# Performance work log

Measured on AMD Instinct MI355X. Metric: run time of the kernel, lower is better.

## Reference

```python
import jax, jax.numpy as jnp
import numpy as np

GROUPS = 8
HEADS = 8
EPS = 1e-5


def setup_inputs() -> dict:
    key = jax.random.key(0)
    ks = jax.random.split(key, 4)
    B, C, T = 4, 512, 2048
    x = jax.random.normal(ks[0], (B, C, T), dtype=jnp.float32)
    gn_w = jnp.ones((C,), dtype=jnp.float32)
    gn_b = jnp.zeros((C,), dtype=jnp.float32)
    qkv_w = jax.random.normal(ks[1], (3 * C, C), dtype=jnp.float32) * (1.0 / np.sqrt(C))
    qkv_b = jnp.zeros((3 * C,), dtype=jnp.float32)
    proj_w = jax.random.normal(ks[2], (C, C), dtype=jnp.float32) * (1.0 / np.sqrt(C))
    proj_b = jnp.zeros((C,), dtype=jnp.float32)
    return {"x": x, "gn_w": gn_w, "gn_b": gn_b, "qkv_w": qkv_w,
            "qkv_b": qkv_b, "proj_w": proj_w, "proj_b": proj_b}


def reference(x, gn_w, gn_b, qkv_w, qkv_b, proj_w, proj_b):
    b, c, t = x.shape
    # GroupNorm over (channels_in_group, T)
    xg = x.reshape(b, GROUPS, c // GROUPS, t)
    mean = xg.mean(axis=(2, 3), keepdims=True)
    var = xg.var(axis=(2, 3), keepdims=True)
    h = ((xg - mean) * jax.lax.rsqrt(var + EPS)).reshape(b, c, t)
    h = h * gn_w[None, :, None] + gn_b[None, :, None]
    # 1x1 conv qkv: [b, 3c, t]
    qkv = jnp.einsum('oc,bct->bot', qkv_w, h) + qkv_b[None, :, None]
    # split into heads: legacy layout [b*H, 3*ch, t] -> q,k,v each [b*H, ch, t]
    ch = c // HEADS
    qkv = qkv.reshape(b * HEADS, 3 * ch, t)
    q, k, v = qkv[:, :ch], qkv[:, ch:2 * ch], qkv[:, 2 * ch:]
    scale = 1.0 / np.sqrt(np.sqrt(ch))
    weight = jnp.einsum('bct,bcs->bts', q * scale, k * scale)  # [bH, t, t]
    weight = jax.nn.softmax(weight.astype(jnp.float32), axis=-1).astype(q.dtype)
    a = jnp.einsum('bts,bcs->bct', weight, v).reshape(b, c, t)
    # 1x1 conv proj
    out = jnp.einsum('oc,bct->bot', proj_w, a) + proj_b[None, :, None]
    return x + out
```

## Files before the change

kernel.cpp:

```cpp
#include <hip/hip_runtime.h>


typedef __attribute__((ext_vector_type(8))) short short8;
typedef __attribute__((ext_vector_type(4))) float f32x4;
typedef __attribute__((ext_vector_type(16))) float f32x16;

#define T_DIM 2048
#define C_DIM 512
#define B_DIM 4

__device__ __forceinline__ float bf2f(ushort u) {
  union { unsigned int i; float f; } x; x.i = ((unsigned int)u) << 16; return x.f;
}
__device__ __forceinline__ ushort f2bf(float f) {
  union { float f; unsigned int i; } x; x.f = f;
  unsigned int i = x.i;
  return (ushort)((i + 0x7FFFu + ((i >> 16) & 1u)) >> 16);
}
__device__ __forceinline__ unsigned int cvtpk_bf16(float lo, float hi) {
  unsigned int r;
  asm("v_cvt_pk_bf16_f32 %0, %1, %2" : "=v"(r) : "v"(lo), "v"(hi));
  return r;
}
__device__ __forceinline__ float exp2_raw(float x) {
  float r;
  asm("v_exp_f32 %0, %1" : "=v"(r) : "v"(x));
  return r;
}
__device__ __forceinline__ void gl_lds16(const ushort* g, const ushort* l) {
  __builtin_amdgcn_global_load_lds(
      (const __attribute__((address_space(1))) unsigned int*)g,
      (__attribute__((address_space(3))) unsigned int*)l, 16, 0, 0);
}

#define KT_SCALE 0.1803368801f

__global__ __launch_bounds__(256) void prep_kernel(
    const float* __restrict__ qkv_w, ushort* __restrict__ wq,
    const float* __restrict__ proj_w, ushort* __restrict__ wp,
    const float* __restrict__ x, float2* __restrict__ part) {
  const int bi = blockIdx.x;
  const int tid = threadIdx.x;
  if (bi < 1024) {
    const float* s = (bi < 768) ? qkv_w : proj_w;
    ushort* d = (bi < 768) ? wq : wp;
    int i = ((bi < 768) ? bi : bi - 768) * 256 + tid;
    float4 v = ((const float4*)s)[i];
    ushort4 o;
    o.x = f2bf(v.x); o.y = f2bf(v.y); o.z = f2bf(v.z); o.w = f2bf(v.w);
    ((ushort4*)d)[i] = o;
    return;
  }
  const int pb = bi - 1024;
  const float4* p4 = (const float4*)x + (size_t)pb * 2048;
  float s = 0.f, ss = 0.f;
#pragma unroll
  for (int i = 0; i < 8; i++) {
    float4 v = p4[tid + i * 256];
    s += v.x + v.y + v.z + v.w;
    ss += v.x * v.x + v.y * v.y + v.z * v.z + v.w * v.w;
  }
  for (int off = 32; off; off >>= 1) {
    s += __shfl_xor(s, off, 64);
    ss += __shfl_xor(ss, off, 64);
  }
  __shared__ float rbuf[8];
  int w = tid >> 6, lane = tid & 63;
  if (lane == 0) { rbuf[w * 2] = s; rbuf[w * 2 + 1] = ss; }
  __syncthreads();
  if (tid == 0) {
    float S = 0.f, SS = 0.f;
#pragma unroll
    for (int i = 0; i < 4; i++) { S += rbuf[2 * i]; SS += rbuf[2 * i + 1]; }
    part[pb] = make_float2(S, SS);
  }
}

__global__ __launch_bounds__(256) void gn_apply_t_kernel(
    const float* __restrict__ x, const float* __restrict__ gw,
    const float* __restrict__ gb, const float2* __restrict__ part,
    ushort* __restrict__ ht) {
  __shared__ ushort tile[64][66];
  __shared__ float sst[2];
  const int b = blockIdx.z, gy = blockIdx.y, c0 = gy * 64, t0 = blockIdx.x * 64;
  const int tid = threadIdx.x;
  if (tid < 64) {
    float s = 0.f, ss = 0.f;
    if (tid < 16) {
      float2 p = part[(b * 8 + gy) * 16 + tid];
      s = p.x; ss = p.y;
    }
    for (int off = 8; off; off >>= 1) {
      s += __shfl_xor(s, off, 64);
      ss += __shfl_xor(ss, off, 64);
    }
    if (tid == 0) {
      float mean = s * (1.f / 131072.f);
      float var = ss * (1.f / 131072.f) - mean * mean;
      sst[0] = mean;
      sst[1] = rsqrtf(var + 1e-5f);
    }
  }
  __syncthreads();
  const float mean = sst[0], rstd = sst[1];
  {
    const int cc = tid >> 2, tc = (tid & 3) * 16;
    const int c = c0 + cc;
    float sc = rstd * gw[c];
    float bb = gb[c] - mean * sc;
    const float4* src = (const float4*)(x + ((size_t)b * 512 + c) * T_DIM + t0 + tc);
    unsigned int* dst = (unsigned int*)&tile[cc][tc];
#pragma unroll
    for (int q = 0; q < 4; q++) {
      float4 v = src[q];
      float a0 = v.x * sc + bb, a1 = v.y * sc + bb;
      float a2 = v.z * sc + bb, a3 = v.w * sc + bb;
      dst[2 * q] = (unsigned int)f2bf(a0) | ((unsigned int)f2bf(a1) << 16);
      dst[2 * q + 1] = (unsigned int)f2bf(a2) | ((unsigned int)f2bf(a3) << 16);
    }
  }
  __syncthreads();
  {
    const int tt = tid >> 2, ch = (tid & 3) * 16;
    union { uint4 v4[2]; ushort u[16]; } z;
#pragma unroll
    for (int j = 0; j < 16; j++) z.u[j] = tile[ch + j][tt];
    ushort* dst = ht + ((size_t)b * T_DIM + t0 + tt) * 512 + c0 + ch;
    *(uint4*)dst = z.v4[0];
    *(uint4*)(dst + 8) = z.v4[1];
  }
}

template <int MODE, int MF>
__global__ __launch_bounds__(256, 3) void gemm_bt_kernel(
    const ushort* __restrict__ Wb, const ushort* __restrict__ Bt,
    const float* __restrict__ bias, const float* __restrict__ xres,
    ushort* __restrict__ outb, float* __restrict__ outf,
    ushort* __restrict__ ktp, int M) {
  __shared__ ushort As[MF * 32 * 64];
  __shared__ ushort Bs[128 * 64];
  const int b = blockIdx.z;
  const int t0 = blockIdx.x * 128, o0 = blockIdx.y * (MF * 32);
  const int tid = threadIdx.x, lane = tid & 63, w = tid >> 6;
  const int li = lane & 15, g = lane >> 4;
  const int wm = (w >> 1) * (MF * 16), wn = (w & 1) * 64;
  const int r8 = tid >> 3, bl = tid & 7;
  const ushort* Bbase = Bt + (size_t)b * T_DIM * 512;

  f32x4 acc[MF][4];
#pragma unroll
  for (int m = 0; m < MF; m++)
#pragma unroll
    for (int n = 0; n < 4; n++) acc[m][n] = (f32x4){0.f, 0.f, 0.f, 0.f};

  for (int ks = 0; ks < 8; ks++) {
    const int k0 = ks * 64;
#pragma unroll
    for (int i = 0; i < 4; i++) {
      int row = i * 32 + r8;
      int sb = (bl ^ (row & 7)) << 3;
      if (i < MF)
        gl_lds16(Wb + (size_t)(o0 + row) * 512 + k0 + sb, As + row * 64 + bl * 8);
      gl_lds16(Bbase + (size_t)(t0 + row) * 512 + k0 + sb, Bs + row * 64 + bl * 8);
    }
    __syncthreads();
#pragma unroll
    for (int kk = 0; kk < 2; kk++) {
      short8 af[MF], bf[4];
#pragma unroll
      for (int m = 0; m < MF; m++)
        af[m] = *(const short8*)&As[(wm + m * 16 + li) * 64 +
                                    (((kk * 4 + g) ^ (li & 7)) << 3)];
#pragma unroll
      for (int n = 0; n < 4; n++)
        bf[n] = *(const short8*)&Bs[(wn + n * 16 + li) * 64 +
                                    (((kk * 4 + g) ^ (li & 7)) << 3)];
      __builtin_amdgcn_s_setprio(1);
#pragma unroll
      for (int m = 0; m < MF; m++)
#pragma unroll
        for (int n = 0; n < 4; n++)
          acc[m][n] = __builtin_amdgcn_mfma_f32_16x16x32_bf16(af[m], bf[n],
                                                              acc[m][n], 0, 0, 0);
      __builtin_amdgcn_s_setprio(0);
    }
    __syncthreads();
  }

  size_t obase = (size_t)b * M * T_DIM;
#pragma unroll
  for (int m = 0; m < MF; m++) {
    const int om = o0 + wm + m * 16;
    bool isK = false;
    int head = 0, rem0 = 0;
    if (MODE == 0) {
      head = om / 192;
      rem0 = om - head * 192;
      isK = (rem0 >= 64 && rem0 < 128);
    }
    if (MODE == 0 && isK) {
      const int d0 = rem0 - 64 + g * 4;
      const size_t ktbase = (size_t)(b * 8 + head) * T_DIM;
      float bv0 = bias[om + g * 4 + 0];
      float bv1 = bias[om + g * 4 + 1];
      float bv2 = bias[om + g * 4 + 2];
      float bv3 = bias[om + g * 4 + 3];
#pragma unroll
      for (int n = 0; n < 4; n++) {
        int t = t0 + wn + n * 16 + li;
        ushort4 kv;
        kv.x = f2bf(KT_SCALE * (acc[m][n][0] + bv0));
        kv.y = f2bf(KT_SCALE * (acc[m][n][1] + bv1));
        kv.z = f2bf(KT_SCALE * (acc[m][n][2] + bv2));
        kv.w = f2bf(KT_SCALE * (acc[m][n][3] + bv3));
        *(ushort4*)(ktp + (ktbase + t) * 64 + d0) = kv;
      }
    } else {
#pragma unroll
      for (int r = 0; r < 4; r++) {
        int o = om + g * 4 + r;
        float bv = bias[o];
#pragma unroll
        for (int n = 0; n < 4; n++) {
          int t = t0 + wn + n * 16 + li;
          float v = acc[m][n][r] + bv;
          size_t idx = obase + (size_t)o * T_DIM + t;
          if (MODE == 0) outb[idx] = f2bf(v);
          else outf[idx] = v + xres[idx];
        }
      }
    }
  }
}

__global__ __launch_bounds__(256, 4) void attn_part_kernel(
    const ushort* __restrict__ qkv, const ushort* __restrict__ Ktg,
    ushort* __restrict__ opart, float* __restrict__ lpart) {
  __shared__ ushort SH[16384];
  const int bh = blockIdx.x, b = bh >> 3, hh = bh & 7;
  const int ttile = blockIdx.y;
  const int t0 = ttile * 128;
  const int shalf = blockIdx.z;
  const int tid = threadIdx.x, lane = tid & 63, w = tid >> 6;
  const int tl = lane & 31, hi = lane >> 5;
  const size_t base = ((size_t)b * 1536 + hh * 192) * (size_t)T_DIM;
  const ushort* Qp = qkv + base;
  const ushort* Vp = qkv + base + (size_t)128 * T_DIM + shalf * 1024;
  const ushort* Kp = Ktg + (size_t)bh * T_DIM * 64 + (size_t)shalf * 1024 * 64;
  const int tcol = t0 + w * 32 + tl;

  short8 qb[4];
#pragma unroll
  for (int kc = 0; kc < 4; kc++) {
    union { short8 s; ushort u[8]; } tmp;
#pragma unroll
    for (int j = 0; j < 8; j++)
      tmp.u[j] = Qp[(size_t)(kc * 16 + hi * 8 + j) * T_DIM + tcol];
    qb[kc] = tmp.s;
  }

  const int srow = lane >> 3;
  const int sblk = (lane & 7) ^ srow;

  const ushort* kg = Kp + (size_t)(w * 16 + srow) * 64 + sblk * 8;
  const ushort* vg = Vp + (size_t)(w * 16 + srow) * T_DIM + sblk * 8;
  const int ldW = w * 1024;

  f32x16 zv;
#pragma unroll
  for (int r = 0; r < 16; r++) zv[r] = 0.f;
  f32x16 oacc0, oacc1;
#pragma unroll
  for (int r = 0; r < 16; r++) { oacc0[r] = 0.f; oacc1[r] = 0.f; }
  float lsum = 0.f;

  gl_lds16(kg, SH + ldW);
  gl_lds16(kg + 512, SH + ldW + 512);
  gl_lds16(vg, SH + 8192 + ldW);
  gl_lds16(vg + 8 * T_DIM, SH + 8192 + ldW + 512);
  kg += 4096;
  vg += 64;

#define CHUNK(BUF, PF)                                                        \
  {                                                                           \
    __syncthreads();                                                          \
    if (PF) {                                                                 \
      gl_lds16(kg, SH + ((BUF) ^ 1) * 4096 + ldW);                            \
      gl_lds16(kg + 512, SH + ((BUF) ^ 1) * 4096 + ldW + 512);                \
      gl_lds16(vg, SH + 8192 + ((BUF) ^ 1) * 4096 + ldW);                     \
      gl_lds16(vg + 8 * T_DIM, SH + 8192 + ((BUF) ^ 1) * 4096 + ldW + 512);   \
      kg += 4096;                                                             \
      vg += 64;                                                               \
    }                                                                         \
    const ushort* kb = SH + (BUF) * 4096;                                     \
    const ushort* vb = SH + 8192 + (BUF) * 4096;                              \
    f32x16 s0, s1;                                                            \
    __builtin_amdgcn_s_setprio(1);                                            \
    _Pragma("unroll") for (int kc = 0; kc < 4; kc++) {                        \
      const int bo = (((kc * 2 + hi) ^ (tl & 7)) << 3);                       \
      short8 ak0 = *(const short8*)&kb[tl * 64 + bo];                         \
      short8 ak1 = *(const short8*)&kb[(32 + tl) * 64 + bo];                  \
      s0 = __builtin_amdgcn_mfma_f32_32x32x16_bf16(ak0, qb[kc],               \
                                                   kc == 0 ? zv : s0, 0, 0, 0);\
      s1 = __builtin_amdgcn_mfma_f32_32x32x16_bf16(ak1, qb[kc],               \
                                                   kc == 0 ? zv : s1, 0, 0, 0);\
    }                                                                         \
    __builtin_amdgcn_s_setprio(0);                                            \
    _Pragma("unroll") for (int r = 0; r < 16; r++) {                          \
      s0[r] = exp2_raw(s0[r]);                                                \
      s1[r] = exp2_raw(s1[r]);                                                \
    }                                                                         \
    {                                                                         \
      float a0 = (s0[0] + s0[1]) + (s0[2] + s0[3]);                           \
      float a1 = (s0[4] + s0[5]) + (s0[6] + s0[7]);                           \
      float a2 = (s0[8] + s0[9]) + (s0[10] + s0[11]);                         \
      float a3 = (s0[12] + s0[13]) + (s0[14] + s0[15]);                       \
      float b0 = (s1[0] + s1[1]) + (s1[2] + s1[3]);                           \
      float b1 = (s1[4] + s1[5]) + (s1[6] + s1[7]);                           \
      float b2 = (s1[8] + s1[9]) + (s1[10] + s1[11]);                         \
      float b3 = (s1[12] + s1[13]) + (s1[14] + s1[15]);                       \
      lsum += ((a0 + a1) + (a2 + a3)) + ((b0 + b1) + (b2 + b3));              \
    }                                                                         \
    unsigned int pw[2][8];                                                    \
    _Pragma("unroll") for (int p = 0; p < 8; p++) {                           \
      pw[0][p] = cvtpk_bf16(s0[2 * p], s0[2 * p + 1]);                        \
      pw[1][p] = cvtpk_bf16(s1[2 * p], s1[2 * p + 1]);                        \
    }                                                                         \
    short8 bp[4];                                                             \
    _Pragma("unroll") for (int kc = 0; kc < 4; kc++) {                        \
      const int n = kc >> 1, q = (kc & 1) * 4;                                \
      union { short8 s; unsigned int wv[4]; } bu;                             \
      _Pragma("unroll") for (int h = 0; h < 2; h++) {                         \
        unsigned int P0 = pw[n][q + h];                                       \
        unsigned int P1 = pw[n][q + 2 + h];                                   \
        asm volatile("v_permlane32_swap_b32 %0, %1" : "+v"(P0), "+v"(P1));    \
        bu.wv[h] = P0;                                                        \
        bu.wv[2 + h] = P1;                                                    \
      }                                                                       \
      bp[kc] = bu.s;                                                          \
    }                                                                         \
    __builtin_amdgcn_s_setprio(1);                                            \
    _Pragma("unroll") for (int kc = 0; kc < 4; kc++) {                        \
      const int bo = (((kc * 2 + hi) ^ (tl & 7)) << 3);                       \
      short8 av0 = *(const short8*)&vb[tl * 64 + bo];                         \
      short8 av1 = *(const short8*)&vb[(32 + tl) * 64 + bo];                  \
      oacc0 = __builtin_amdgcn_mfma_f32_32x32x16_bf16(av0, bp[kc], oacc0,     \
                                                      0, 0, 0);               \
      oacc1 = __builtin_amdgcn_mfma_f32_32x32x16_bf16(av1, bp[kc], oacc1,     \
                                                      0, 0, 0);               \
    }                                                                         \
    __builtin_amdgcn_s_setprio(0);                                            \
  }

  for (int cc = 0; cc < 8; cc++) {
    CHUNK(0, true);
    CHUNK(1, cc < 7);
  }
#undef CHUNK

  const int pidx = (bh * 16 + ttile) * 2 + shalf;
  ushort* op = opart + (size_t)pidx * 8192;
#pragma unroll
  for (int r = 0; r < 16; r++) {
    int crow = (r & 3) + 8 * (r >> 2) + 4 * hi;
    op[crow * 128 + w * 32 + tl] = f2bf(oacc0[r]);
    op[(32 + crow) * 128 + w * 32 + tl] = f2bf(oacc1[r]);
  }
  float lrow = lsum + __shfl_xor(lsum, 32);
  if (hi == 0) lpart[(size_t)pidx * 128 + w * 32 + tl] = lrow;
}

__global__ __launch_bounds__(256) void combine_kernel(
    const ushort* __restrict__ opart, const float* __restrict__ lpart,
    ushort* __restrict__ at) {
  __shared__ float invl[128];
  __shared__ ushort tile[128][66];
  const int bh = blockIdx.x, ttile = blockIdx.y, b = bh >> 3, hh = bh & 7;
  const int tid = threadIdx.x;
  const size_t pb = (size_t)(bh * 16 + ttile) * 2;
  const float* l0 = lpart + pb * 128;
  if (tid < 128) invl[tid] = 1.f / (l0[tid] + l0[128 + tid]);
  __syncthreads();
  {
    const int c = tid & 63, seg = tid >> 6;
    const ushort* r0 = opart + pb * 8192 + c * 128 + seg * 32;
    union { uint4 v[4]; ushort u[32]; } x0, x1;
#pragma unroll
    for (int j = 0; j < 4; j++) {
      x0.v[j] = *(const uint4*)(r0 + j * 8);
      x1.v[j] = *(const uint4*)(r0 + 8192 + j * 8);
    }
#pragma unroll
    for (int j = 0; j < 32; j++) {
      int t = seg * 32 + j;
      tile[t][c] = f2bf((bf2f(x0.u[j]) + bf2f(x1.u[j])) * invl[t]);
    }
  }
  __syncthreads();
  {
    const int t = tid >> 1, ch = (tid & 1) * 32;
    union { uint4 v[4]; ushort u[32]; } z;
#pragma unroll
    for (int j = 0; j < 32; j++) z.u[j] = tile[t][ch + j];
    uint4* dst = (uint4*)(at + ((size_t)b * T_DIM + ttile * 128 + t) * 512 +
                          hh * 64 + ch);
#pragma unroll
    for (int j = 0; j < 4; j++) dst[j] = z.v[j];
  }
}

extern "C" void kernel_launch(void* const* d_in, const int* in_sizes, int n_in,
                              void* d_out, int out_size, void* d_ws,
                              size_t ws_size, hipStream_t stream) {
  const float* x = (const float*)d_in[0];
  const float* gn_w = (const float*)d_in[1];
  const float* gn_b = (const float*)d_in[2];
  const float* qkv_w = (const float*)d_in[3];
  const float* qkv_b = (const float*)d_in[4];
  const float* proj_w = (const float*)d_in[5];
  const float* proj_b = (const float*)d_in[6];
  float* out = (float*)d_out;

  char* ws = (char*)d_ws;
  float2* part = (float2*)ws;
  ushort* ht_bf = (ushort*)(ws + 8192);
  ushort* at_bf = ht_bf;
  ushort* qkv_bf = (ushort*)(ws + 8192 + 8388608);
  ushort* wq_bf = (ushort*)(ws + 8192 + 8388608 + 25165824);
  ushort* wp_bf = (ushort*)(ws + 8192 + 8388608 + 25165824 + 1572864);
  ushort* kt_bf = (ushort*)(ws + 8192 + 8388608 + 25165824 + 1572864 + 524288);
  ushort* op_bf = (ushort*)(ws + 8192 + 8388608 + 25165824 + 1572864 + 524288 +
                            8388608);
  float* lp_f = (float*)(ws + 8192 + 8388608 + 25165824 + 1572864 + 524288 +
                         8388608 + 16777216);

  prep_kernel<<<1536, 256, 0, stream>>>(qkv_w, wq_bf, proj_w, wp_bf, x, part);
  gn_apply_t_kernel<<<dim3(32, 8, 4), 256, 0, stream>>>(x, gn_w, gn_b, part, ht_bf);
  gemm_bt_kernel<0, 4><<<dim3(16, 12, 4), 256, 0, stream>>>(
      wq_bf, ht_bf, qkv_b, nullptr, qkv_bf, nullptr, kt_bf, 1536);
  attn_part_kernel<<<dim3(32, 16, 2), 256, 0, stream>>>(qkv_bf, kt_bf, op_bf, lp_f);
  combine_kernel<<<dim3(32, 16), 256, 0, stream>>>(op_bf, lp_f, at_bf);
  gemm_bt_kernel<1, 2><<<dim3(16, 8, 4), 256, 0, stream>>>(
      wp_bf, at_bf, proj_b, x, nullptr, out, nullptr, 512);
}
```

Before: 96.97 us.

## Software-pipeline QK^T of next chunk with softmax and PV of previous chunk

Restructures the attention inner loop so that each iteration computes the S=K·Q MFMAs for chunk C, then runs exp, row sum, bf16 packing and the PV MFMAs for chunk C-1. V gets a triple-buffered LDS ring so the previous chunk's V stays valid while the next one is prefetched. The aim is to overlap MFMA work with the exp and permlane VALU work. In exchange it holds two sets of score accumulators live, which raises register pressure, and it enlarges LDS, so launch bounds drop from 4 to 3 blocks per CU.

```diff
diff --git a/kernel.cpp b/kernel.cpp
--- a/kernel.cpp
+++ b/kernel.cpp
@@ -233,10 +233,10 @@
   }
 }
 
-__global__ __launch_bounds__(256, 4) void attn_part_kernel(
+__global__ __launch_bounds__(256, 3) void attn_part_kernel(
     const ushort* __restrict__ qkv, const ushort* __restrict__ Ktg,
     ushort* __restrict__ opart, float* __restrict__ lpart) {
-  __shared__ ushort SH[16384];
+  __shared__ ushort SH[20480];
   const int bh = blockIdx.x, b = bh >> 3, hh = bh & 7;
   const int ttile = blockIdx.y;
   const int t0 = ttile * 128;
@@ -273,6 +273,7 @@
 #pragma unroll
   for (int r = 0; r < 16; r++) { oacc0[r] = 0.f; oacc1[r] = 0.f; }
   float lsum = 0.f;
+  f32x16 sA0, sA1, sB0, sB1;
 
   gl_lds16(kg, SH + ldW);
   gl_lds16(kg + 512, SH + ldW + 512);
@@ -281,50 +282,27 @@
   kg += 4096;
   vg += 64;
 
-#define CHUNK(BUF, PF)                                                        \
+#define SMPV(C, S)                                                            \
   {                                                                           \
-    __syncthreads();                                                          \
-    if (PF) {                                                                 \
-      gl_lds16(kg, SH + ((BUF) ^ 1) * 4096 + ldW);                            \
-      gl_lds16(kg + 512, SH + ((BUF) ^ 1) * 4096 + ldW + 512);                \
-      gl_lds16(vg, SH + 8192 + ((BUF) ^ 1) * 4096 + ldW);                     \
-      gl_lds16(vg + 8 * T_DIM, SH + 8192 + ((BUF) ^ 1) * 4096 + ldW + 512);   \
-      kg += 4096;                                                             \
-      vg += 64;                                                               \
-    }                                                                         \
-    const ushort* kb = SH + (BUF) * 4096;                                     \
-    const ushort* vb = SH + 8192 + (BUF) * 4096;                              \
-    f32x16 s0, s1;                                                            \
-    __builtin_amdgcn_s_setprio(1);                                            \
-    _Pragma("unroll") for (int kc = 0; kc < 4; kc++) {                        \
-      const int bo = (((kc * 2 + hi) ^ (tl & 7)) << 3);                       \
-      short8 ak0 = *(const short8*)&kb[tl * 64 + bo];                         \
-      short8 ak1 = *(const short8*)&kb[(32 + tl) * 64 + bo];                  \
-      s0 = __builtin_amdgcn_mfma_f32_32x32x16_bf16(ak0, qb[kc],               \
-                                                   kc == 0 ? zv : s0, 0, 0, 0);\
-      s1 = __builtin_amdgcn_mfma_f32_32x32x16_bf16(ak1, qb[kc],               \
-                                                   kc == 0 ? zv : s1, 0, 0, 0);\
-    }                                                                         \
-    __builtin_amdgcn_s_setprio(0);                                            \
     _Pragma("unroll") for (int r = 0; r < 16; r++) {                          \
-      s0[r] = exp2_raw(s0[r]);                                                \
-      s1[r] = exp2_raw(s1[r]);                                                \
+      S##0[r] = exp2_raw(S##0[r]);                                            \
+      S##1[r] = exp2_raw(S##1[r]);                                            \
     }                                                                         \
     {                                                                         \
-      float a0 = (s0[0] + s0[1]) + (s0[2] + s0[3]);                           \
-      float a1 = (s0[4] + s0[5]) + (s0[6] + s0[7]);                           \
-      float a2 = (s0[8] + s0[9]) + (s0[10] + s0[11]);                         \
-      float a3 = (s0[12] + s0[13]) + (s0[14] + s0[15]);                       \
-      float b0 = (s1[0] + s1[1]) + (s1[2] + s1[3]);                           \
-      float b1 = (s1[4] + s1[5]) + (s1[6] + s1[7]);                           \
-      float b2 = (s1[8] + s1[9]) + (s1[10] + s1[11]);                         \
-      float b3 = (s1[12] + s1[13]) + (s1[14] + s1[15]);                       \
+      float a0 = (S##0[0] + S##0[1]) + (S##0[2] + S##0[3]);                   \
+      float a1 = (S##0[4] + S##0[5]) + (S##0[6] + S##0[7]);                   \
+      float a2 = (S##0[8] + S##0[9]) + (S##0[10] + S##0[11]);                 \
+      float a3 = (S##0[12] + S##0[13]) + (S##0[14] + S##0[15]);               \
+      float b0 = (S##1[0] + S##1[1]) + (S##1[2] + S##1[3]);                   \
+      float b1 = (S##1[4] + S##1[5]) + (S##1[6] + S##1[7]);                   \
+      float b2 = (S##1[8] + S##1[9]) + (S##1[10] + S##1[11]);                 \
+      float b3 = (S##1[12] + S##1[13]) + (S##1[14] + S##1[15]);               \
       lsum += ((a0 + a1) + (a2 + a3)) + ((b0 + b1) + (b2 + b3));              \
     }                                                                         \
     unsigned int pw[2][8];                                                    \
     _Pragma("unroll") for (int p = 0; p < 8; p++) {                           \
-      pw[0][p] = cvtpk_bf16(s0[2 * p], s0[2 * p + 1]);                        \
-      pw[1][p] = cvtpk_bf16(s1[2 * p], s1[2 * p + 1]);                        \
+      pw[0][p] = cvtpk_bf16(S##0[2 * p], S##0[2 * p + 1]);                    \
+      pw[1][p] = cvtpk_bf16(S##1[2 * p], S##1[2 * p + 1]);                    \
     }                                                                         \
     short8 bp[4];                                                             \
     _Pragma("unroll") for (int kc = 0; kc < 4; kc++) {                        \
@@ -339,6 +317,7 @@
       }                                                                       \
       bp[kc] = bu.s;                                                          \
     }                                                                         \
+    const ushort* vb = SH + 8192 + (((C) % 3)) * 4096;                        \
     __builtin_amdgcn_s_setprio(1);                                            \
     _Pragma("unroll") for (int kc = 0; kc < 4; kc++) {                        \
       const int bo = (((kc * 2 + hi) ^ (tl & 7)) << 3);                       \
@@ -352,11 +331,53 @@
     __builtin_amdgcn_s_setprio(0);                                            \
   }
 
-  for (int cc = 0; cc < 8; cc++) {
-    CHUNK(0, true);
-    CHUNK(1, cc < 7);
-  }
-#undef CHUNK
+#define ITER(C, SN, SO)                                                       \
+  {                                                                           \
+    __syncthreads();                                                          \
+    if ((C) < 15) {                                                           \
+      gl_lds16(kg, SH + (((C) + 1) & 1) * 4096 + ldW);                        \
+      gl_lds16(kg + 512, SH + (((C) + 1) & 1) * 4096 + ldW + 512);            \
+      gl_lds16(vg, SH + 8192 + (((C) + 1) % 3) * 4096 + ldW);                 \
+      gl_lds16(vg + 8 * T_DIM, SH + 8192 + (((C) + 1) % 3) * 4096 + ldW + 512); \
+      kg += 4096;                                                             \
+      vg += 64;                                                               \
+    }                                                                         \
+    {                                                                         \
+      const ushort* kb = SH + ((C) & 1) * 4096;                               \
+      __builtin_amdgcn_s_setprio(1);                                          \
+      _Pragma("unroll") for (int kc = 0; kc < 4; kc++) {                      \
+        const int bo = (((kc * 2 + hi) ^ (tl & 7)) << 3);                     \
+        short8 ak0 = *(const short8*)&kb[tl * 64 + bo];                       \
+        short8 ak1 = *(const short8*)&kb[(32 + tl) * 64 + bo];                \
+        SN##0 = __builtin_amdgcn_mfma_f32_32x32x16_bf16(                      \
+            ak0, qb[kc], kc == 0 ? zv : SN##0, 0, 0, 0);                      \
+        SN##1 = __builtin_amdgcn_mfma_f32_32x32x16_bf16(                      \
+            ak1, qb[kc], kc == 0 ? zv : SN##1, 0, 0, 0);                      \
+      }                                                                       \
+      __builtin_amdgcn_s_setprio(0);                                          \
+    }                                                                         \
+    if ((C) > 0) SMPV((C) - 1, SO)                                            \
+  }
+
+  ITER(0, sA, sB);
+  ITER(1, sB, sA);
+  ITER(2, sA, sB);
+  ITER(3, sB, sA);
+  ITER(4, sA, sB);
+  ITER(5, sB, sA);
+  ITER(6, sA, sB);
+  ITER(7, sB, sA);
+  ITER(8, sA, sB);
+  ITER(9, sB, sA);
+  ITER(10, sA, sB);
+  ITER(11, sB, sA);
+  ITER(12, sA, sB);
+  ITER(13, sB, sA);
+  ITER(14, sA, sB);
+  ITER(15, sB, sA);
+  SMPV(15, sB)
+#undef ITER
+#undef SMPV
 
   const int pidx = (bh * 16 + ttile) * 2 + shalf;
   ushort* op = opart + (size_t)pidx * 8192;
```

New measurement: 100.1 us. +3.2%, slower.
